# Kernel optimization log

Measured on AMD Instinct MI355X. Metric: run time of the kernel, lower is better.

## Reference

```python
import jax, jax.numpy as jnp
import numpy as np

N_TOK, TOKDIM = 2048, 1024
NHEADS, KDIM = 16, 64


def setup_inputs() -> dict:
    key = jax.random.key(0)
    kg, kk, kq = jax.random.split(key, 3)
    g = jax.random.normal(kg, (N_TOK, TOKDIM), dtype=jnp.float32)
    # params use normal(stddev=0.002) init, as in the flax module
    Wk = 0.002 * jax.random.normal(kk, (NHEADS, KDIM, TOKDIM), dtype=jnp.float32)
    Wq = 0.002 * jax.random.normal(kq, (NHEADS, KDIM, TOKDIM), dtype=jnp.float32)
    return {"g": g, "Wk": Wk, "Wq": Wq}


def reference(g, Wk, Wq):
    """manual_grad of the attention energy: returns d(energy)/dg, shape [n, d]."""
    H, Z, D = Wk.shape
    betas = jnp.full((H,), 1.0, dtype=g.dtype) / jnp.sqrt(jnp.asarray(Z, g.dtype))
    K = jnp.einsum('hzd,kd->khz', Wk, g)   # [n,h,z]
    Q = jnp.einsum('hzd,qd->qhz', Wq, g)   # [n,h,z]
    F1 = jnp.einsum('hzd,khz->khd', Wq, K)  # [n,h,d]
    F2 = jnp.einsum('hzd,qhz->qhd', Wk, Q)  # [n,h,d]
    A1 = jnp.einsum('h,khz,qhz->hqk', betas, K, Q)  # [h,q,k] scores
    A2 = jax.nn.softmax(A1, -1)
    T1 = -jnp.einsum('khd,hqk->qd', F1, A2)
    T2 = -jnp.einsum('qhd,hqk->kd', F2, A2)
    return T1 + T2
```

## Files before the change

kernel.cpp:

```cpp
#include <hip/hip_runtime.h>
#include <stdint.h>

#define NT 2048
#define TD 1024
#define NH 16
static constexpr float SCL = 0.18033688011112042f;

typedef __attribute__((ext_vector_type(8))) short bf16x8;
typedef __attribute__((ext_vector_type(4))) float f32x4;
typedef __attribute__((address_space(3))) uint32_t lds_u32;
typedef __attribute__((address_space(1))) uint32_t glb_u32;

__device__ __forceinline__ float bf2f(unsigned short u){
  union { uint32_t u32; float f; } v; v.u32 = ((uint32_t)u) << 16; return v.f;
}
__device__ __forceinline__ unsigned short f2bf(float f){
  union { float f; uint32_t u; } v; v.f = f;
  uint32_t r = v.u + 0x7fffu + ((v.u >> 16) & 1u);
  return (unsigned short)(r >> 16);
}
__device__ __forceinline__ bf16x8 ld8(const unsigned short* base, int row, int kc){
  return *(const bf16x8*)((const char*)base + row*128 + ((kc ^ (row & 7)) << 4));
}
__device__ __forceinline__ bf16x8 ld16(const unsigned short* base, int row, int kc){
  return *(const bf16x8*)((const char*)base + row*256 + ((kc ^ (row & 15)) << 4));
}
template<int N> __device__ __forceinline__ void wait_vm_lgkm0(){
  if constexpr (N == 0)      asm volatile("s_waitcnt vmcnt(0) lgkmcnt(0)" ::: "memory");
  else if constexpr (N == 4) asm volatile("s_waitcnt vmcnt(4) lgkmcnt(0)" ::: "memory");
  else if constexpr (N == 6) asm volatile("s_waitcnt vmcnt(6) lgkmcnt(0)" ::: "memory");
  __builtin_amdgcn_sched_barrier(0);
}

__global__ __launch_bounds__(256) void prep_kernel(
    const float* __restrict__ g, const float* __restrict__ Wk, const float* __restrict__ Wq,
    unsigned short* __restrict__ gbf, unsigned short* __restrict__ wkq,
    unsigned short* __restrict__ twqk)
{
  int b = blockIdx.x;
  if (b < 1024) {
    int base = b * 2048 + threadIdx.x;
    #pragma unroll
    for (int i = 0; i < 8; i++) { int idx = base + i * 256; gbf[idx] = f2bf(g[idx]); }
  } else if (b < 2048) {
    int base = (b - 1024) * 2048 + threadIdx.x;
    #pragma unroll
    for (int i = 0; i < 8; i++) {
      int idx = base + i * 256;
      float v = (idx < (1 << 20)) ? Wk[idx] : Wq[idx - (1 << 20)];
      wkq[idx] = f2bf(v);
    }
  } else {
    int t = b - 2048;
    int dt = t & 31, jt = t >> 5;
    __shared__ float tile[32][33];
    int tx = threadIdx.x & 31, ty = threadIdx.x >> 5;
    int j0 = jt * 32, d0 = dt * 32;
    const float* src = (j0 < 1024) ? Wq : Wk;
    int jb = (j0 < 1024) ? j0 : (j0 - 1024);
    #pragma unroll
    for (int rr = 0; rr < 4; rr++)
      tile[ty + rr * 8][tx] = src[(size_t)(jb + ty + rr * 8) * 1024 + d0 + tx];
    __syncthreads();
    #pragma unroll
    for (int rr = 0; rr < 4; rr++)
      twqk[(size_t)(d0 + ty + rr * 8) * 2048 + j0 + tx] = f2bf(tile[tx][ty + rr * 8]);
  }
}

__global__ __launch_bounds__(256) void qst_kernel(const unsigned short* __restrict__ tkq,
                                                  const float* __restrict__ L,
                                                  unsigned short* __restrict__ qst)
{
  int r = blockIdx.x;
  int h = r >> 6;
  const unsigned short* src = tkq + (size_t)(1024 + r) * 2048;
  unsigned short* dst = qst + (size_t)r * 2048;
  const float* Lh = L + (size_t)h * NT;
  for (int q = threadIdx.x; q < NT; q += 256)
    dst[q] = f2bf(bf2f(src[q]) / Lh[q]);
}

template<int TM, int TN, int EPI, int WPE>
__global__ __launch_bounds__(256, WPE) void btg2_kernel(
    const unsigned short* __restrict__ A, int lda,
    const unsigned short* __restrict__ BT, int ldb,
    int Kdim, void* C0, void* C1)
{
  constexpr int WM = TM / 2, WN = TN / 2, FM = WM / 16, FN = WN / 16;
  constexpr int AC = TM / 32, BC = TN / 32, LOADS = AC + BC;
  __shared__ __align__(16) unsigned short As[3][TM * 64];
  __shared__ __align__(16) unsigned short Bs[3][TN * 64];
  int tid = threadIdx.x, lane = tid & 63, wave = tid >> 6;
  int wr = wave >> 1, wc = wave & 1, lrow = lane & 15, g = lane >> 4;
  int bm = blockIdx.x * TM, bn = blockIdx.y * TN;

  auto stage = [&](unsigned short* bufA, unsigned short* bufB, int kk) {
    #pragma unroll
    for (int i = 0; i < AC; i++) {
      int c = i * 256 + tid, row = c >> 3, sl = ((c & 7) ^ (row & 7)) << 3;
      __builtin_amdgcn_global_load_lds((glb_u32*)(A + (size_t)(bm + row) * lda + kk + sl),
          (lds_u32*)((char*)bufA + i * 4096 + wave * 1024), 16, 0, 0);
    }
    #pragma unroll
    for (int i = 0; i < BC; i++) {
      int c = i * 256 + tid, row = c >> 3, sl = ((c & 7) ^ (row & 7)) << 3;
      __builtin_amdgcn_global_load_lds((glb_u32*)(BT + (size_t)(bn + row) * ldb + kk + sl),
          (lds_u32*)((char*)bufB + i * 4096 + wave * 1024), 16, 0, 0);
    }
  };

  f32x4 acc[FM][FN] = {};
  int nt = Kdim >> 6;
  stage(As[0], Bs[0], 0);
  stage(As[1], Bs[1], 64);
  wait_vm_lgkm0<LOADS>();
  __builtin_amdgcn_s_barrier();
  int bc = 0;
  for (int t = 0; t < nt; t++) {
    int bp = bc + 2; if (bp >= 3) bp -= 3;
    if (t + 2 < nt) stage(As[bp], Bs[bp], (t + 2) * 64);
    const unsigned short* Ac = As[bc];
    const unsigned short* Bc = Bs[bc];
    #pragma unroll
    for (int k2 = 0; k2 < 2; k2++) {
      bf16x8 a_[FM], b_[FN];
      #pragma unroll
      for (int m = 0; m < FM; m++) a_[m] = ld8(Ac, wr * WM + m * 16 + lrow, k2 * 4 + g);
      #pragma unroll
      for (int n = 0; n < FN; n++) b_[n] = ld8(Bc, wc * WN + n * 16 + lrow, k2 * 4 + g);
      #pragma unroll
      for (int m = 0; m < FM; m++)
        #pragma unroll
        for (int n = 0; n < FN; n++)
          acc[m][n] = __builtin_amdgcn_mfma_f32_16x16x32_bf16(a_[m], b_[n], acc[m][n], 0, 0, 0);
    }
    if (t + 2 < nt) wait_vm_lgkm0<LOADS>(); else wait_vm_lgkm0<0>();
    __builtin_amdgcn_s_barrier();
    bc = (bc == 2) ? 0 : bc + 1;
  }
  #pragma unroll
  for (int m = 0; m < FM; m++) {
    int rb = bm + wr * WM + m * 16 + 4 * g;
    #pragma unroll
    for (int n = 0; n < FN; n++) {
      int cc = bn + wc * WN + n * 16 + lrow;
      f32x4 v = acc[m][n];
      if constexpr (EPI == 0) {
        unsigned short* Cp = (unsigned short*)C0;
        unsigned short* T  = (unsigned short*)C1;
        float sc = (bn < 1024) ? SCL : 1.0f;
        unsigned short pt[4];
        #pragma unroll
        for (int j = 0; j < 4; j++) {
          pt[j] = f2bf(v[j]);
          Cp[(size_t)(rb + j) * 2048 + cc] = f2bf(v[j] * sc);
        }
        ushort4 t4; t4.x = pt[0]; t4.y = pt[1]; t4.z = pt[2]; t4.w = pt[3];
        *(ushort4*)(T + (size_t)cc * 2048 + rb) = t4;
      } else {
        float* Cf = (float*)C0;
        #pragma unroll
        for (int j = 0; j < 4; j++) Cf[(size_t)(rb + j) * 1024 + cc] = -v[j];
      }
    }
  }
}

template<bool DIV>
__global__ __launch_bounds__(512, 4) void fused_kernel(
    const unsigned short* __restrict__ CKQ,
    const unsigned short* __restrict__ AUXT,
    unsigned short* __restrict__ C,
    float* __restrict__ Lg)
{
  __shared__ __align__(16) char pool[81920];
  unsigned short* PB = (unsigned short*)(pool + 65536);
  float* Red   = (float*)pool;
  float* L_lds = (float*)(pool + 32768);

  int tid = threadIdx.x, lane = tid & 63, wave = tid >> 6;
  int wr = wave >> 2, wcq = wave & 3, lrow = lane & 15, g = lane >> 4;
  int p0 = blockIdx.x * 64, h = blockIdx.y, h64 = h * 64;
  int cA = DIV ? h64 : TD + h64;
  int cB = DIV ? TD + h64 : h64;
  const unsigned short* AuxG = AUXT + (size_t)h64 * 2048;

  auto stageAin = [&](char* dst, int i0) {
    #pragma unroll
    for (int i = 0; i < 2; i++) {
      int c = i * 512 + tid, row = c >> 3, scol = ((c & 7) ^ (row & 7)) << 3;
      __builtin_amdgcn_global_load_lds((glb_u32*)(CKQ + (size_t)(i0 + row) * 2048 + cA + scol),
          (lds_u32*)(dst + i * 8192 + wave * 1024), 16, 0, 0);
    }
  };
  auto stageAux = [&](char* dst, int i0) {
    #pragma unroll
    for (int i = 0; i < 2; i++) {
      int c = i * 512 + tid, row = c >> 4, scol = ((c & 15) ^ (row & 15)) << 3;
      __builtin_amdgcn_global_load_lds((glb_u32*)(AuxG + (size_t)row * 2048 + i0 + scol),
          (lds_u32*)(dst + i * 8192 + wave * 1024), 16, 0, 0);
    }
  };

  { int row = tid >> 3, scol = ((tid & 7) ^ (row & 7)) << 3;
    __builtin_amdgcn_global_load_lds((glb_u32*)(CKQ + (size_t)(p0 + row) * 2048 + cB + scol),
        (lds_u32*)((char*)PB + wave * 1024), 16, 0, 0); }
  stageAin(pool, 0);
  stageAux(pool + 32768, 0);
  wait_vm_lgkm0<0>();
  __builtin_amdgcn_s_barrier();

  bf16x8 bs[2];
  #pragma unroll
  for (int k2 = 0; k2 < 2; k2++)
    bs[k2] = ld8(PB, wcq * 16 + lrow, k2 * 4 + g);
  __syncthreads();

  unsigned short* PldsW = (unsigned short*)(pool + 65536 + wave * 2048);
  f32x4 acc_pv[4] = {};
  float lsum = 0.f;

  for (int t = 0; t < 16; t++) {
    const unsigned short* curA = (const unsigned short*)(pool + (t & 1) * 16384);
    const unsigned short* curX = (const unsigned short*)(pool + 32768 + (t & 1) * 16384);
    if (t + 1 < 16) {
      stageAin(pool + ((t + 1) & 1) * 16384, (t + 1) * 128);
      stageAux(pool + 32768 + ((t + 1) & 1) * 16384, (t + 1) * 128);
    }
    f32x4 acc_s[4] = {};
    __builtin_amdgcn_s_setprio(1);
    #pragma unroll
    for (int k2 = 0; k2 < 2; k2++) {
      bf16x8 a_[4];
      #pragma unroll
      for (int m = 0; m < 4; m++) a_[m] = ld8(curA, wr * 64 + m * 16 + lrow, k2 * 4 + g);
      #pragma unroll
      for (int m = 0; m < 4; m++)
        acc_s[m] = __builtin_amdgcn_mfma_f32_16x16x32_bf16(a_[m], bs[k2], acc_s[m], 0, 0, 0);
    }
    __builtin_amdgcn_s_setprio(0);
    #pragma unroll
    for (int m = 0; m < 4; m++) {
      float e0 = exp2f(acc_s[m][0]);
      float e1 = exp2f(acc_s[m][1]);
      float e2 = exp2f(acc_s[m][2]);
      float e3 = exp2f(acc_s[m][3]);
      if (DIV) lsum += (e0 + e1) + (e2 + e3);
      uint32_t lo, hi;
      asm("v_cvt_pk_bf16_f32 %0, %1, %2" : "=v"(lo) : "v"(e0), "v"(e1));
      asm("v_cvt_pk_bf16_f32 %0, %1, %2" : "=v"(hi) : "v"(e2), "v"(e3));
      uint2 wv; wv.x = lo; wv.y = hi;
      int slot = m * 2 + (g >> 1);
      *(uint2*)((char*)PldsW + lrow * 128 + ((slot ^ (lrow & 7)) << 4) + (g & 1) * 8) = wv;
    }
    asm volatile("s_waitcnt lgkmcnt(0)" ::: "memory");
    __builtin_amdgcn_sched_barrier(0);
    __builtin_amdgcn_s_setprio(1);
    #pragma unroll
    for (int k2p = 0; k2p < 2; k2p++) {
      bf16x8 pa = ld8(PldsW, lrow, k2p * 4 + g);
      #pragma unroll
      for (int n4 = 0; n4 < 4; n4++) {
        bf16x8 pb = ld16(curX, n4 * 16 + lrow, wr * 8 + k2p * 4 + g);
        acc_pv[n4] = __builtin_amdgcn_mfma_f32_16x16x32_bf16(pa, pb, acc_pv[n4], 0, 0, 0);
      }
    }
    __builtin_amdgcn_s_setprio(0);
    wait_vm_lgkm0<0>();
    __builtin_amdgcn_s_barrier();
  }

  #pragma unroll
  for (int n4 = 0; n4 < 4; n4++)
    #pragma unroll
    for (int j = 0; j < 4; j++)
      Red[(size_t)(wr * 64 + wcq * 16 + 4 * g + j) * 64 + n4 * 16 + lrow] = acc_pv[n4][j];
  if (DIV && tid < 64) L_lds[tid] = 0.f;
  __syncthreads();
  if (DIV) {
    lsum += __shfl_xor(lsum, 16); lsum += __shfl_xor(lsum, 32);
    if (lane < 16) atomicAdd(&L_lds[wcq * 16 + lane], lsum);
    __syncthreads();
    if (tid < 64) Lg[(size_t)h * NT + p0 + tid] = L_lds[tid];
  }
  int p = tid >> 3, zb = (tid & 7) * 8;
  float inv = DIV ? 1.0f / L_lds[p] : 1.0f;
  int cbase = DIV ? h64 : TD + h64;
  unsigned short ob[8];
  #pragma unroll
  for (int zz = 0; zz < 8; zz += 4) {
    f32x4 s0 = *(f32x4*)&Red[(size_t)(0 * 64 + p) * 64 + zb + zz];
    f32x4 s1 = *(f32x4*)&Red[(size_t)(1 * 64 + p) * 64 + zb + zz];
    #pragma unroll
    for (int j = 0; j < 4; j++) ob[zz + j] = f2bf((s0[j] + s1[j]) * inv);
  }
  unsigned short* dst = C + (size_t)(p0 + p) * 2048 + cbase + zb;
  *(ushort4*)dst = *(ushort4*)&ob[0];
  *(ushort4*)(dst + 4) = *(ushort4*)&ob[4];
}

extern "C" void kernel_launch(void* const* d_in, const int* in_sizes, int n_in,
                              void* d_out, int out_size, void* d_ws, size_t ws_size,
                              hipStream_t stream)
{
  (void)in_sizes; (void)n_in; (void)out_size; (void)ws_size;
  const float* g  = (const float*)d_in[0];
  const float* Wk = (const float*)d_in[1];
  const float* Wq = (const float*)d_in[2];

  char* ws = (char*)d_ws;
  size_t off = 0;
  auto alloc = [&](size_t b) -> char* {
    char* p = ws + off; off += (b + 255) & ~((size_t)255); return p;
  };
  unsigned short* gbf  = (unsigned short*)alloc((size_t)NT * TD * 2);
  unsigned short* wkq  = (unsigned short*)alloc((size_t)2 * TD * TD * 2);
  unsigned short* twqk = (unsigned short*)alloc((size_t)TD * 2048 * 2);
  unsigned short* CKQ  = (unsigned short*)alloc((size_t)NT * 2048 * 2);
  unsigned short* TKQ  = (unsigned short*)alloc((size_t)NT * 2048 * 2);
  unsigned short* CB12 = (unsigned short*)alloc((size_t)NT * 2048 * 2);
  unsigned short* QsT  = (unsigned short*)alloc((size_t)TD * NT * 2);
  float*          Lbuf = (float*)alloc((size_t)NH * NT * 4);

  prep_kernel<<<dim3(4096), dim3(256), 0, stream>>>(g, Wk, Wq, gbf, wkq, twqk);

  btg2_kernel<128, 64, 0, 2><<<dim3(16, 32), dim3(256), 0, stream>>>(
      gbf, TD, wkq, TD, TD, (void*)CKQ, (void*)TKQ);

  fused_kernel<true><<<dim3(32, NH), dim3(512), 0, stream>>>(CKQ, TKQ, CB12, Lbuf);

  qst_kernel<<<dim3(1024), dim3(256), 0, stream>>>(TKQ, Lbuf, QsT);

  fused_kernel<false><<<dim3(32, NH), dim3(512), 0, stream>>>(CKQ, QsT, CB12, nullptr);

  btg2_kernel<64, 64, 4, 3><<<dim3(32, 16), dim3(256), 0, stream>>>(
      CB12, 2048, twqk, 2048, 2048, d_out, nullptr);
}
```

Baseline: 120.6 us.

## Switch fused attention kernel to 32x32x16 MFMA with register-resident probabilities

Replaces the 16x16x32 MFMA tiling in the fused kernel with 32x32x16 MFMAs over a 4x2 wave grid. Each wave keeps its exp'd score tile in registers as the A operand of the PV product, which removes the per-iteration LDS write, wait and reload of probabilities. The epilogue now reduces across four waves and writes single bf16 values per thread instead of vectorised stores, and LDS use drops. The trade-offs are more register pressure from 16-wide accumulators, possible extra bank conflicts on the split 8-byte B loads, and less coalesced output stores.

```diff
diff --git a/kernel.cpp b/kernel.cpp
--- a/kernel.cpp
+++ b/kernel.cpp
@@ -8,6 +8,7 @@
 
 typedef __attribute__((ext_vector_type(8))) short bf16x8;
 typedef __attribute__((ext_vector_type(4))) float f32x4;
+typedef __attribute__((ext_vector_type(16))) float f32x16;
 typedef __attribute__((address_space(3))) uint32_t lds_u32;
 typedef __attribute__((address_space(1))) uint32_t glb_u32;
 
@@ -21,9 +22,6 @@
 }
 __device__ __forceinline__ bf16x8 ld8(const unsigned short* base, int row, int kc){
   return *(const bf16x8*)((const char*)base + row*128 + ((kc ^ (row & 7)) << 4));
-}
-__device__ __forceinline__ bf16x8 ld16(const unsigned short* base, int row, int kc){
-  return *(const bf16x8*)((const char*)base + row*256 + ((kc ^ (row & 15)) << 4));
 }
 template<int N> __device__ __forceinline__ void wait_vm_lgkm0(){
   if constexpr (N == 0)      asm volatile("s_waitcnt vmcnt(0) lgkmcnt(0)" ::: "memory");
@@ -174,13 +172,14 @@
     unsigned short* __restrict__ C,
     float* __restrict__ Lg)
 {
-  __shared__ __align__(16) char pool[81920];
+  __shared__ __align__(16) char pool[73984];
   unsigned short* PB = (unsigned short*)(pool + 65536);
   float* Red   = (float*)pool;
-  float* L_lds = (float*)(pool + 32768);
+  float* L_lds = (float*)(pool + 73728);
 
   int tid = threadIdx.x, lane = tid & 63, wave = tid >> 6;
-  int wr = wave >> 2, wcq = wave & 3, lrow = lane & 15, g = lane >> 4;
+  int wr = wave >> 1, wc = wave & 1;
+  int zr = lane & 31, hi = lane >> 5;
   int p0 = blockIdx.x * 64, h = blockIdx.y, h64 = h * 64;
   int cA = DIV ? h64 : TD + h64;
   int cB = DIV ? TD + h64 : h64;
@@ -208,96 +207,115 @@
         (lds_u32*)((char*)PB + wave * 1024), 16, 0, 0); }
   stageAin(pool, 0);
   stageAux(pool + 32768, 0);
+  if (DIV && tid < 64) L_lds[tid] = 0.f;
   wait_vm_lgkm0<0>();
   __builtin_amdgcn_s_barrier();
 
-  bf16x8 bs[2];
-  #pragma unroll
-  for (int k2 = 0; k2 < 2; k2++)
-    bs[k2] = ld8(PB, wcq * 16 + lrow, k2 * 4 + g);
-  __syncthreads();
-
-  unsigned short* PldsW = (unsigned short*)(pool + 65536 + wave * 2048);
-  f32x4 acc_pv[4] = {};
+  bf16x8 bs[4];
+  #pragma unroll
+  for (int kz = 0; kz < 4; kz++)
+    bs[kz] = ld8(PB, wc * 32 + zr, 2 * kz + hi);
+
+  int aoff[4];
+  #pragma unroll
+  for (int kz = 0; kz < 4; kz++) {
+    int row = wr * 32 + zr;
+    aoff[kz] = row * 128 + (((2 * kz + hi) ^ (row & 7)) << 4);
+  }
+  int boff[2][2][2];
+  #pragma unroll
+  for (int zb = 0; zb < 2; zb++)
+    #pragma unroll
+    for (int ks = 0; ks < 2; ks++)
+      #pragma unroll
+      for (int d = 0; d < 2; d++) {
+        int zrow = zb * 32 + zr;
+        int l = 4 * wr + 2 * ks + d;
+        boff[zb][ks][d] = zrow * 256 + ((l ^ (zrow & 15)) << 4) + hi * 8;
+      }
+
+  f32x16 acc_pv[2] = {};
   float lsum = 0.f;
 
   for (int t = 0; t < 16; t++) {
-    const unsigned short* curA = (const unsigned short*)(pool + (t & 1) * 16384);
-    const unsigned short* curX = (const unsigned short*)(pool + 32768 + (t & 1) * 16384);
+    const char* curA = pool + (t & 1) * 16384;
+    const char* curX = pool + 32768 + (t & 1) * 16384;
     if (t + 1 < 16) {
       stageAin(pool + ((t + 1) & 1) * 16384, (t + 1) * 128);
       stageAux(pool + 32768 + ((t + 1) & 1) * 16384, (t + 1) * 128);
     }
-    f32x4 acc_s[4] = {};
+    f32x16 acc_s = {};
     __builtin_amdgcn_s_setprio(1);
     #pragma unroll
-    for (int k2 = 0; k2 < 2; k2++) {
-      bf16x8 a_[4];
-      #pragma unroll
-      for (int m = 0; m < 4; m++) a_[m] = ld8(curA, wr * 64 + m * 16 + lrow, k2 * 4 + g);
-      #pragma unroll
-      for (int m = 0; m < 4; m++)
-        acc_s[m] = __builtin_amdgcn_mfma_f32_16x16x32_bf16(a_[m], bs[k2], acc_s[m], 0, 0, 0);
+    for (int kz = 0; kz < 4; kz++) {
+      bf16x8 a_ = *(const bf16x8*)(curA + aoff[kz]);
+      acc_s = __builtin_amdgcn_mfma_f32_32x32x16_bf16(a_, bs[kz], acc_s, 0, 0, 0);
     }
     __builtin_amdgcn_s_setprio(0);
-    #pragma unroll
-    for (int m = 0; m < 4; m++) {
-      float e0 = exp2f(acc_s[m][0]);
-      float e1 = exp2f(acc_s[m][1]);
-      float e2 = exp2f(acc_s[m][2]);
-      float e3 = exp2f(acc_s[m][3]);
-      if (DIV) lsum += (e0 + e1) + (e2 + e3);
-      uint32_t lo, hi;
-      asm("v_cvt_pk_bf16_f32 %0, %1, %2" : "=v"(lo) : "v"(e0), "v"(e1));
-      asm("v_cvt_pk_bf16_f32 %0, %1, %2" : "=v"(hi) : "v"(e2), "v"(e3));
-      uint2 wv; wv.x = lo; wv.y = hi;
-      int slot = m * 2 + (g >> 1);
-      *(uint2*)((char*)PldsW + lrow * 128 + ((slot ^ (lrow & 7)) << 4) + (g & 1) * 8) = wv;
-    }
-    asm volatile("s_waitcnt lgkmcnt(0)" ::: "memory");
-    __builtin_amdgcn_sched_barrier(0);
+    float ev[16];
+    #pragma unroll
+    for (int r = 0; r < 16; r++) ev[r] = exp2f(acc_s[r]);
+    if (DIV) {
+      #pragma unroll
+      for (int r = 0; r < 16; r++) lsum += ev[r];
+    }
+    union { bf16x8 v; uint32_t w[4]; } pu[2];
+    #pragma unroll
+    for (int ks = 0; ks < 2; ks++)
+      #pragma unroll
+      for (int i = 0; i < 4; i++)
+        asm("v_cvt_pk_bf16_f32 %0, %1, %2"
+            : "=v"(pu[ks].w[i]) : "v"(ev[8 * ks + 2 * i]), "v"(ev[8 * ks + 2 * i + 1]));
     __builtin_amdgcn_s_setprio(1);
     #pragma unroll
-    for (int k2p = 0; k2p < 2; k2p++) {
-      bf16x8 pa = ld8(PldsW, lrow, k2p * 4 + g);
-      #pragma unroll
-      for (int n4 = 0; n4 < 4; n4++) {
-        bf16x8 pb = ld16(curX, n4 * 16 + lrow, wr * 8 + k2p * 4 + g);
-        acc_pv[n4] = __builtin_amdgcn_mfma_f32_16x16x32_bf16(pa, pb, acc_pv[n4], 0, 0, 0);
+    for (int zb = 0; zb < 2; zb++)
+      #pragma unroll
+      for (int ks = 0; ks < 2; ks++) {
+        union { bf16x8 v; uint2 u[2]; } bb;
+        bb.u[0] = *(const uint2*)(curX + boff[zb][ks][0]);
+        bb.u[1] = *(const uint2*)(curX + boff[zb][ks][1]);
+        acc_pv[zb] = __builtin_amdgcn_mfma_f32_32x32x16_bf16(pu[ks].v, bb.v, acc_pv[zb], 0, 0, 0);
       }
-    }
     __builtin_amdgcn_s_setprio(0);
     wait_vm_lgkm0<0>();
     __builtin_amdgcn_s_barrier();
   }
 
   #pragma unroll
-  for (int n4 = 0; n4 < 4; n4++)
-    #pragma unroll
-    for (int j = 0; j < 4; j++)
-      Red[(size_t)(wr * 64 + wcq * 16 + 4 * g + j) * 64 + n4 * 16 + lrow] = acc_pv[n4][j];
-  if (DIV && tid < 64) L_lds[tid] = 0.f;
+  for (int zb = 0; zb < 2; zb++) {
+    int z = zb * 32 + zr;
+    #pragma unroll
+    for (int u = 0; u < 4; u++) {
+      int p = wc * 32 + 8 * u + 4 * hi;
+      f32x4 q;
+      q[0] = acc_pv[zb][4 * u]; q[1] = acc_pv[zb][4 * u + 1];
+      q[2] = acc_pv[zb][4 * u + 2]; q[3] = acc_pv[zb][4 * u + 3];
+      *(f32x4*)&Red[(size_t)(wr * 64 + z) * 64 + p] = q;
+    }
+  }
+  if (DIV) {
+    lsum += __shfl_xor(lsum, 32);
+    if (hi == 0) atomicAdd(&L_lds[wc * 32 + zr], lsum);
+  }
   __syncthreads();
-  if (DIV) {
-    lsum += __shfl_xor(lsum, 16); lsum += __shfl_xor(lsum, 32);
-    if (lane < 16) atomicAdd(&L_lds[wcq * 16 + lane], lsum);
-    __syncthreads();
-    if (tid < 64) Lg[(size_t)h * NT + p0 + tid] = L_lds[tid];
-  }
-  int p = tid >> 3, zb = (tid & 7) * 8;
-  float inv = DIV ? 1.0f / L_lds[p] : 1.0f;
+  if (DIV && tid < 64) Lg[(size_t)h * NT + p0 + tid] = L_lds[tid];
+  int z = tid & 63, pg = tid >> 6;
+  float s[8] = {0.f, 0.f, 0.f, 0.f, 0.f, 0.f, 0.f, 0.f};
+  #pragma unroll
+  for (int w2 = 0; w2 < 4; w2++) {
+    f32x4 x0 = *(f32x4*)&Red[(size_t)(w2 * 64 + z) * 64 + pg * 8];
+    f32x4 x1 = *(f32x4*)&Red[(size_t)(w2 * 64 + z) * 64 + pg * 8 + 4];
+    #pragma unroll
+    for (int j = 0; j < 4; j++) { s[j] += x0[j]; s[4 + j] += x1[j]; }
+  }
   int cbase = DIV ? h64 : TD + h64;
-  unsigned short ob[8];
-  #pragma unroll
-  for (int zz = 0; zz < 8; zz += 4) {
-    f32x4 s0 = *(f32x4*)&Red[(size_t)(0 * 64 + p) * 64 + zb + zz];
-    f32x4 s1 = *(f32x4*)&Red[(size_t)(1 * 64 + p) * 64 + zb + zz];
-    #pragma unroll
-    for (int j = 0; j < 4; j++) ob[zz + j] = f2bf((s0[j] + s1[j]) * inv);
-  }
-  unsigned short* dst = C + (size_t)(p0 + p) * 2048 + cbase + zb;
-  *(ushort4*)dst = *(ushort4*)&ob[0];
-  *(ushort4*)(dst + 4) = *(ushort4*)&ob[4];
+  #pragma unroll
+  for (int i = 0; i < 8; i++) {
+    int p = pg * 8 + i;
+    float x = s[i];
+    if (DIV) x /= L_lds[p];
+    C[(size_t)(p0 + p) * 2048 + cbase + z] = f2bf(x);
+  }
 }
 
 extern "C" void kernel_launch(void* const* d_in, const int* in_sizes, int n_in,
```

Result: slower. 125.5 us (+4.1%).
